# Kernel optimization log

Measured on AMD Instinct MI355X. Metric: run time of the kernel, lower is better.

## Reference

```python
import jax, jax.numpy as jnp
import numpy as np

BS, N, D, NC = 64, 512, 256, 4
REG = 0.5
N_ITER = 10
BIG = 1.0e9
LN_EPS = 1e-5


def _layer_norm(x, g, b):
    m = jnp.mean(x, axis=-1, keepdims=True)
    v = jnp.mean((x - m) ** 2, axis=-1, keepdims=True)
    return (x - m) * jax.lax.rsqrt(v + LN_EPS) * g + b


def _embed(x, W1, b1, g1, be1, W2, b2, g2, be2):
    h = _layer_norm(jax.nn.leaky_relu(x @ W1 + b1, 0.01), g1, be1)
    return _layer_norm(jax.nn.leaky_relu(h @ W2 + b2, 0.01), g2, be2)


def _one_hot_st(logits):
    # convert_one_hot(mode='max', hard=True, four_class=False, train): straight-through one-hot
    y = jax.nn.softmax(logits, axis=-1)
    y_hard = jax.nn.one_hot(jnp.argmax(y, axis=-1), logits.shape[-1], dtype=y.dtype)
    return jax.lax.stop_gradient(y_hard - y) + y


def _cdist(x, y):
    # torch.cdist p=2 (matmul form)
    sq = (jnp.sum(x * x, -1)[:, :, None] + jnp.sum(y * y, -1)[:, None, :]
          - 2.0 * jnp.einsum('bnd,bmd->bnm', x, y))
    return jnp.sqrt(jnp.maximum(sq, 0.0))


def _sinkhorn(a, b, C):
    # standard Sinkhorn-Knopp (POT sinkhorn_knopp), reg=REG, maxIter=N_ITER
    K = jnp.exp(-C / REG)
    def step(carry, _):
        u, v = carry
        v = b / (K.T @ u)
        u = a / (K @ v)
        return (u, v), None
    init = (jnp.full_like(a, 1.0 / a.shape[0]), jnp.full_like(b, 1.0 / b.shape[0]))
    (u, v), _ = jax.lax.scan(step, init, None, length=N_ITER)
    return u[:, None] * K * v[None, :]


def setup_inputs() -> dict:
    ks = jax.random.split(jax.random.key(0), 8)
    sc = 1.0 / np.sqrt(D)
    return {
        'case_A_logits': jax.random.normal(ks[0], (BS, N, NC), jnp.float32),
        'case_B_logits': jax.random.normal(ks[1], (BS, N, NC), jnp.float32),
        'case_A': jax.random.normal(ks[2], (BS, N, D), jnp.float32),
        'case_B': jax.random.normal(ks[3], (BS, N, D), jnp.float32),
        'relation_matrix': jax.random.uniform(ks[4], (BS, N, N), jnp.float32),
        'padding_mask_a': jnp.ones((BS, N), jnp.float32),
        'padding_mask_b': jnp.ones((BS, N), jnp.float32),
        'W1': jax.random.normal(ks[5], (D, D), jnp.float32) * sc,
        'b1': jnp.zeros((D,), jnp.float32),
        'g1': jnp.ones((D,), jnp.float32),
        'be1': jnp.zeros((D,), jnp.float32),
        'W2': jax.random.normal(ks[6], (D, D), jnp.float32) * sc,
        'b2': jnp.zeros((D,), jnp.float32),
        'g2': jnp.ones((D,), jnp.float32),
        'be2': jnp.zeros((D,), jnp.float32),
    }


def reference(case_A_logits, case_B_logits, case_A, case_B, relation_matrix,
              padding_mask_a, padding_mask_b,
              W1, b1, g1, be1, W2, b2, g2, be2):
    n = case_B_logits.shape[1]
    A1 = _one_hot_st(case_A_logits)                       # [bs, n, 4]
    B1 = _one_hot_st(case_B_logits)
    class_mask = jnp.einsum('bnc,bmc->bnm', A1, B1)       # [bs, n, n]
    pm = padding_mask_a[:, :, None] * padding_mask_b[:, None, :]
    pmv = -BIG * pm + BIG
    eA = _embed(case_A, W1, b1, g1, be1, W2, b2, g2, be2)
    eB = _embed(case_B, W1, b1, g1, be1, W2, b2, g2, be2)
    cost = _cdist(eA, eB)                                 # [bs, n, n]
    cost_class = cost + pmv                               # train path
    margin = jnp.full((n,), 1.0 / n, cost.dtype)
    plan = jax.vmap(lambda c: _sinkhorn(margin, margin, c))(cost_class)
    in_loss = jnp.mean(cost_class * class_mask * pm)
    out_loss = -jnp.mean(cost_class * (1.0 - class_mask) * pm)
    # simot branch: MSE criterion, simpercent=1.0 -> sim_mask all ones
    loss_raw = (plan * n - relation_matrix) ** 2
    sup_loss = jnp.sum(loss_raw * padding_mask_a[:, :, None]) / jnp.sum(padding_mask_a)
    return in_loss + out_loss + 10.0 * sup_loss
```

## Files before the change

### kernel.cpp

```cpp
#include <hip/hip_runtime.h>
#include <math.h>

#define BSZ 64
#define NPTS 512
#define DIM 256
#define MROWS 32768
#define TOTROWS 65536
#define BIGF 1.0e9f

typedef __bf16 bf16x8 __attribute__((ext_vector_type(8)));
typedef float  f32x4  __attribute__((ext_vector_type(4)));
typedef __attribute__((address_space(1))) const void* as1cv;
typedef __attribute__((address_space(3))) void* as3v;

#define KB_OFF    0ull
#define X_OFF     8388608ull
#define H_OFF     16777216ull
#define NORM_OFF  25165824ull
#define U_OFF     25231360ull
#define V_OFF     25264128ull
#define ARGA_OFF  25296896ull
#define ARGB_OFF  25329664ull
#define ACC_OFF   25362432ull
#define WT1_OFF   25362944ull
#define WT2_OFF   25395712ull

#define ACC_PA   0
#define ACC_IN   1
#define ACC_SUP  65
#define ACC_CNT  321

__device__ __forceinline__ float bf2f(unsigned short h) {
    return __uint_as_float(((unsigned int)h) << 16);
}
__device__ __forceinline__ unsigned short f2bf(float f) {
    unsigned int u = __float_as_uint(f);
    u = (u + 0x7FFFu + ((u >> 16) & 1u)) >> 16;
    return (unsigned short)u;
}

__device__ __forceinline__ float block_reduce_256(float val) {
    __shared__ float sh[4];
    int lane = threadIdx.x & 63;
    int wv = threadIdx.x >> 6;
    __syncthreads();
#pragma unroll
    for (int off = 32; off > 0; off >>= 1) val += __shfl_down(val, off, 64);
    if (lane == 0) sh[wv] = val;
    __syncthreads();
    float r = 0.f;
    if (wv == 0 && lane < 4) r = sh[lane];
    if (wv == 0) {
        r += __shfl_down(r, 2, 64);
        r += __shfl_down(r, 1, 64);
    }
    return r;
}

__device__ __forceinline__ void unpack8(uint4 w, float* k) {
    k[0] = __uint_as_float(w.x << 16);
    k[1] = __uint_as_float(w.x & 0xFFFF0000u);
    k[2] = __uint_as_float(w.y << 16);
    k[3] = __uint_as_float(w.y & 0xFFFF0000u);
    k[4] = __uint_as_float(w.z << 16);
    k[5] = __uint_as_float(w.z & 0xFFFF0000u);
    k[6] = __uint_as_float(w.w << 16);
    k[7] = __uint_as_float(w.w & 0xFFFF0000u);
}
__device__ __forceinline__ float dot8(const float* k, const float* vr) {
    float rs = k[0] * vr[0];
    rs = fmaf(k[1], vr[1], rs); rs = fmaf(k[2], vr[2], rs);
    rs = fmaf(k[3], vr[3], rs); rs = fmaf(k[4], vr[4], rs);
    rs = fmaf(k[5], vr[5], rs); rs = fmaf(k[6], vr[6], rs);
    return fmaf(k[7], vr[7], rs);
}

__device__ __forceinline__ float packed_reduce4(float p0, float p1, float p2, float p3, int l) {
    p0 += __shfl_xor(p0, 32, 64);
    p1 += __shfl_xor(p1, 32, 64);
    p2 += __shfl_xor(p2, 32, 64);
    p3 += __shfl_xor(p3, 32, 64);
    float m1 = (l & 32) ? p1 : p0;
    float m2 = (l & 32) ? p3 : p2;
    m1 += __shfl_xor(m1, 16, 64);
    m2 += __shfl_xor(m2, 16, 64);
    float s = (l & 16) ? m2 : m1;
    s += __shfl_xor(s, 8, 64);
    s += __shfl_xor(s, 4, 64);
    s += __shfl_xor(s, 2, 64);
    s += __shfl_xor(s, 1, 64);
    return s;
}
__device__ __forceinline__ float bcast_lane(float x, int lane) {
    return __uint_as_float((unsigned)__builtin_amdgcn_readlane((int)__float_as_uint(x), lane));
}

__global__ void zero_acc_kernel(float* acc, float* colsum) {
    int t = blockIdx.x * 256 + threadIdx.x;
    if (t < 512) acc[t] = 0.f;
    colsum[t] = 0.f;
}

__global__ __launch_bounds__(256) void argmax_pa_kernel(
    const float* __restrict__ la, const float* __restrict__ lb,
    const float* __restrict__ pa, int* __restrict__ argA, int* __restrict__ argB,
    float* __restrict__ acc) {
    int i = blockIdx.x * 256 + threadIdx.x;
    float4 a = *(const float4*)&la[(size_t)i * 4];
    float av[4] = {a.x, a.y, a.z, a.w};
    int ba = 0; float bv = av[0];
#pragma unroll
    for (int c = 1; c < 4; ++c) if (av[c] > bv) { bv = av[c]; ba = c; }
    argA[i] = ba;
    float4 b = *(const float4*)&lb[(size_t)i * 4];
    float bw[4] = {b.x, b.y, b.z, b.w};
    int bbi = 0; float bm = bw[0];
#pragma unroll
    for (int c = 1; c < 4; ++c) if (bw[c] > bm) { bm = bw[c]; bbi = c; }
    argB[i] = bbi;
    float p = pa[i];
#pragma unroll
    for (int off = 32; off > 0; off >>= 1) p += __shfl_down(p, off, 64);
    if ((threadIdx.x & 63) == 0) atomicAdd(&acc[ACC_PA], p);
}

__global__ __launch_bounds__(256) void cast_bf_kernel(
    const float* __restrict__ src, unsigned short* __restrict__ dst) {
    int tid = blockIdx.x * 256 + threadIdx.x;
#pragma unroll
    for (int k = 0; k < 4; ++k) {
        int i4 = tid + k * 524288;
        float4 v = *(const float4*)&src[(size_t)i4 * 4];
        ushort4 o;
        o.x = f2bf(v.x); o.y = f2bf(v.y); o.z = f2bf(v.z); o.w = f2bf(v.w);
        *(ushort4*)&dst[(size_t)i4 * 4] = o;
    }
}

__global__ __launch_bounds__(256) void cast_wt_kernel(
    const float* __restrict__ W, unsigned short* __restrict__ Wt) {
    __shared__ float tile[16][17];
    int tx = threadIdx.x & 15, ty = threadIdx.x >> 4;
    int bx = blockIdx.x, by = blockIdx.y;
    tile[ty][tx] = W[(size_t)(by * 16 + ty) * 256 + bx * 16 + tx];
    __syncthreads();
    Wt[(size_t)(bx * 16 + ty) * 256 + by * 16 + tx] = f2bf(tile[tx][ty]);
}

__global__ __launch_bounds__(256) void gemm_bf_kernel(
    const unsigned short* __restrict__ X, const unsigned short* __restrict__ Wt,
    unsigned short* __restrict__ Y) {
    __shared__ unsigned short Xs[64 * 40];
    __shared__ unsigned short Ws[256 * 40];
    const int t = threadIdx.x;
    const int L = t & 63, wv = t >> 6;
    const int q = L >> 4, n = L & 15;
    const size_t row0 = (size_t)blockIdx.x * 64;
    f32x4 acc[16];
#pragma unroll
    for (int nt = 0; nt < 16; ++nt) acc[nt] = (f32x4){0.f, 0.f, 0.f, 0.f};

    for (int k0 = 0; k0 < 256; k0 += 32) {
        {
            int r = t >> 2, seg = t & 3;
            *(uint4*)&Xs[r * 40 + seg * 8] =
                *(const uint4*)&X[(row0 + r) * 256 + k0 + seg * 8];
#pragma unroll
            for (int it = 0; it < 4; ++it) {
                int nn = (t >> 2) + it * 64;
                *(uint4*)&Ws[nn * 40 + seg * 8] =
                    *(const uint4*)&Wt[(size_t)nn * 256 + k0 + seg * 8];
            }
        }
        __syncthreads();
        bf16x8 av = *(const bf16x8*)&Xs[(wv * 16 + n) * 40 + q * 8];
#pragma unroll
        for (int nt = 0; nt < 16; ++nt) {
            bf16x8 bv = *(const bf16x8*)&Ws[(nt * 16 + n) * 40 + q * 8];
            acc[nt] = __builtin_amdgcn_mfma_f32_16x16x32_bf16(av, bv, acc[nt], 0, 0, 0);
        }
        __syncthreads();
    }
#pragma unroll
    for (int nt = 0; nt < 16; ++nt)
#pragma unroll
        for (int r = 0; r < 4; ++r) {
            size_t row = row0 + wv * 16 + q * 4 + r;
            Y[row * 256 + nt * 16 + n] = f2bf(acc[nt][r]);
        }
}

__global__ __launch_bounds__(256) void ln_bf_kernel(
    const unsigned short* __restrict__ Yin, unsigned short* __restrict__ Yout,
    const float* __restrict__ bias, const float* __restrict__ gam,
    const float* __restrict__ bet, float* __restrict__ norms) {
    int lane = threadIdx.x & 63;
    int wv = threadIdx.x >> 6;
    size_t row = (size_t)blockIdx.x * 4 + wv;
    ushort4 y4 = *(const ushort4*)&Yin[row * 256 + lane * 4];
    float4 b4 = *(const float4*)&bias[lane * 4];
    float h[4] = {bf2f(y4.x) + b4.x, bf2f(y4.y) + b4.y, bf2f(y4.z) + b4.z, bf2f(y4.w) + b4.w};
#pragma unroll
    for (int e = 0; e < 4; ++e) h[e] = h[e] >= 0.f ? h[e] : 0.01f * h[e];
    float s = h[0] + h[1] + h[2] + h[3];
    float sq = h[0] * h[0] + h[1] * h[1] + h[2] * h[2] + h[3] * h[3];
#pragma unroll
    for (int off = 32; off > 0; off >>= 1) {
        s += __shfl_down(s, off, 64);
        sq += __shfl_down(sq, off, 64);
    }
    s = __shfl(s, 0, 64); sq = __shfl(sq, 0, 64);
    float mean = s * (1.f / 256.f);
    float var = fmaxf(sq * (1.f / 256.f) - mean * mean, 0.f);
    float inv = rsqrtf(var + 1e-5f);
    float4 g4 = *(const float4*)&gam[lane * 4];
    float4 e4 = *(const float4*)&bet[lane * 4];
    float gv[4] = {g4.x, g4.y, g4.z, g4.w};
    float ev[4] = {e4.x, e4.y, e4.z, e4.w};
    ushort4 o4; float nr = 0.f;
    {
        unsigned short ob[4];
#pragma unroll
        for (int e = 0; e < 4; ++e) {
            float o = (h[e] - mean) * inv * gv[e] + ev[e];
            ob[e] = f2bf(o);
            float orr = bf2f(ob[e]);
            nr += orr * orr;
        }
        o4.x = ob[0]; o4.y = ob[1]; o4.z = ob[2]; o4.w = ob[3];
    }
    *(ushort4*)&Yout[row * 256 + lane * 4] = o4;
    if (norms) {
#pragma unroll
        for (int off = 32; off > 0; off >>= 1) nr += __shfl_down(nr, off, 64);
        if (lane == 0) norms[row] = nr;
    }
}

__global__ __launch_bounds__(256) void cost_mfma_kernel(
    const unsigned short* __restrict__ E, const float* __restrict__ norms,
    const int* __restrict__ argA, const int* __restrict__ argB,
    const float* __restrict__ pa, const float* __restrict__ pb,
    unsigned short* __restrict__ Kb16, float* __restrict__ acc,
    float* __restrict__ colsum) {
    __shared__ unsigned short As[64 * 256];
    __shared__ unsigned short Bs[64 * 256];
    const int t = threadIdx.x;
    const int L = t & 63, wv = t >> 6;
    const int q = L >> 4, n = L & 15;
    const int b = blockIdx.z;
    const int i0 = blockIdx.y * 64, j0 = blockIdx.x * 64;
    const unsigned short* eA = E + (size_t)b * 512 * 256;
    const unsigned short* eB = E + (size_t)(32768 + b * 512) * 256;

    {
        const int lrow = L >> 5;
        const int segp = L & 31;
#pragma unroll
        for (int j = 0; j < 8; ++j) {
            int row = wv * 16 + 2 * j + lrow;
            int sseg = segp ^ (row & 7);
            const unsigned short* ga = &eA[(size_t)(i0 + row) * 256 + sseg * 8];
            const unsigned short* gb = &eB[(size_t)(j0 + row) * 256 + sseg * 8];
            __builtin_amdgcn_global_load_lds((as1cv)ga, (as3v)&As[(wv * 16 + 2 * j) * 256],
                                             16, 0, 0);
            __builtin_amdgcn_global_load_lds((as1cv)gb, (as3v)&Bs[(wv * 16 + 2 * j) * 256],
                                             16, 0, 0);
        }
    }
    f32x4 dot[4];
#pragma unroll
    for (int nt = 0; nt < 4; ++nt) dot[nt] = (f32x4){0.f, 0.f, 0.f, 0.f};
    __syncthreads();

    const int rowa = wv * 16 + n;
    const int sw = n & 7;
#pragma unroll
    for (int c = 0; c < 8; ++c) {
        bf16x8 av = *(const bf16x8*)&As[rowa * 256 + (((c * 4 + q) ^ sw) * 8)];
#pragma unroll
        for (int nt = 0; nt < 4; ++nt) {
            int rowb = nt * 16 + n;
            bf16x8 bv = *(const bf16x8*)&Bs[rowb * 256 + (((c * 4 + q) ^ sw) * 8)];
            dot[nt] = __builtin_amdgcn_mfma_f32_16x16x32_bf16(av, bv, dot[nt], 0, 0, 0);
        }
    }

    int base_row = i0 + wv * 16 + q * 4;
    float nA[4], pAr[4]; int cA[4];
#pragma unroll
    for (int rr = 0; rr < 4; ++rr) {
        nA[rr] = norms[b * 512 + base_row + rr];
        pAr[rr] = pa[b * 512 + base_row + rr];
        cA[rr] = argA[b * 512 + base_row + rr];
    }
    float part = 0.f;
    float csnt[4];
#pragma unroll
    for (int nt = 0; nt < 4; ++nt) {
        int col = j0 + nt * 16 + n;
        float nB = norms[32768 + b * 512 + col];
        float pB = pb[b * 512 + col];
        int cB = argB[b * 512 + col];
        float cloc = 0.f;
#pragma unroll
        for (int rr = 0; rr < 4; ++rr) {
            float d2 = nA[rr] + nB - 2.f * dot[nt][rr];
            float c = sqrtf(fmaxf(d2, 0.f));
            float pm = pAr[rr] * pB;
            float cc = c + (BIGF - BIGF * pm);
            float sgn = (cA[rr] == cB) ? 1.f : -1.f;
            part += cc * sgn * pm;
            unsigned short kb = f2bf(expf(-2.f * cc));
            Kb16[((size_t)b * 512 + base_row + rr) * 512 + col] = kb;
            cloc += bf2f(kb);
        }
        csnt[nt] = cloc;
    }
    __syncthreads();
    float* red = (float*)As;
#pragma unroll
    for (int nt = 0; nt < 4; ++nt) {
        float sq2 = csnt[nt];
        sq2 += __shfl_xor(sq2, 16, 64);
        sq2 += __shfl_xor(sq2, 32, 64);
        if (L < 16) red[wv * 64 + nt * 16 + L] = sq2;
    }
    {
        float pw = part;
#pragma unroll
        for (int off = 32; off > 0; off >>= 1) pw += __shfl_down(pw, off, 64);
        if (L == 0) red[256 + wv] = pw;
    }
    __syncthreads();
    if (t < 64)
        atomicAdd(&colsum[(size_t)b * 512 + j0 + t],
                  red[t] + red[64 + t] + red[128 + t] + red[192 + t]);
    if (t == 0)
        atomicAdd(&acc[ACC_IN + b], red[256] + red[257] + red[258] + red[259]);
}

__global__ __launch_bounds__(1024) void sinkhorn_kernel(
    const unsigned short* __restrict__ Kb16, float* u, float* __restrict__ v) {
    const int b = blockIdx.x;
    const unsigned short* Kb = Kb16 + (size_t)b * 262144;
    __shared__ float vv[512];
    __shared__ float cp[16][512];
    const int t = threadIdx.x, wv = t >> 6, l = t & 63;
    const unsigned short* base = Kb + (size_t)(wv * 32) * 512 + l * 8;

    if (t < 512) vv[t] = 1.f / u[(size_t)b * 512 + t];
    __syncthreads();

    for (int it = 1; it <= 9; ++it) {
        float vr[8];
        *(f32x4*)&vr[0] = *(const f32x4*)&vv[l * 8];
        *(f32x4*)&vr[4] = *(const f32x4*)&vv[l * 8 + 4];
        float cs[8];
#pragma unroll
        for (int e = 0; e < 8; ++e) cs[e] = 0.f;
#pragma unroll 2
        for (int g = 0; g < 8; ++g) {
            const unsigned short* gb = base + (size_t)(g * 4) * 512;
            uint4 w0 = *(const uint4*)(gb);
            uint4 w1 = *(const uint4*)(gb + 512);
            uint4 w2 = *(const uint4*)(gb + 1024);
            uint4 w3 = *(const uint4*)(gb + 1536);
            float k0[8], k1[8], k2[8], k3[8];
            unpack8(w0, k0); unpack8(w1, k1); unpack8(w2, k2); unpack8(w3, k3);
            float p0 = dot8(k0, vr);
            float p1 = dot8(k1, vr);
            float p2 = dot8(k2, vr);
            float p3 = dot8(k3, vr);
            float s = packed_reduce4(p0, p1, p2, p3, l);
            float us = 0.001953125f * __builtin_amdgcn_rcpf(s);
            float uA = bcast_lane(us, 0);
            float uC = bcast_lane(us, 16);
            float uB = bcast_lane(us, 32);
            float uD = bcast_lane(us, 48);
#pragma unroll
            for (int e = 0; e < 8; ++e) {
                float c = fmaf(k0[e], uA, cs[e]);
                c = fmaf(k1[e], uB, c);
                c = fmaf(k2[e], uC, c);
                cs[e] = fmaf(k3[e], uD, c);
            }
        }
        *(f32x4*)&cp[wv][l * 8]     = *(f32x4*)&cs[0];
        *(f32x4*)&cp[wv][l * 8 + 4] = *(f32x4*)&cs[4];
        __syncthreads();
        if (t < 512) {
            float ss = 0.f;
#pragma unroll
            for (int k = 0; k < 16; ++k) ss += cp[k][t];
            vv[t] = (1.f / 512.f) / ss;
        }
        __syncthreads();
    }

    {
        float vr[8];
        *(f32x4*)&vr[0] = *(const f32x4*)&vv[l * 8];
        *(f32x4*)&vr[4] = *(const f32x4*)&vv[l * 8 + 4];
#pragma unroll 2
        for (int g = 0; g < 8; ++g) {
            const unsigned short* gb = base + (size_t)(g * 4) * 512;
            uint4 w0 = *(const uint4*)(gb);
            uint4 w1 = *(const uint4*)(gb + 512);
            uint4 w2 = *(const uint4*)(gb + 1024);
            uint4 w3 = *(const uint4*)(gb + 1536);
            float k0[8], k1[8], k2[8], k3[8];
            unpack8(w0, k0); unpack8(w1, k1); unpack8(w2, k2); unpack8(w3, k3);
            float p0 = dot8(k0, vr);
            float p1 = dot8(k1, vr);
            float p2 = dot8(k2, vr);
            float p3 = dot8(k3, vr);
            float s = packed_reduce4(p0, p1, p2, p3, l);
            if ((l & 15) == 0) {
                int g16 = l >> 4;
                int rof = ((g16 & 1) << 1) | (g16 >> 1);
                u[(size_t)b * 512 + wv * 32 + g * 4 + rof] = 0.001953125f / s;
            }
        }
    }
    if (t < 512) v[(size_t)b * 512 + t] = vv[t];
}

__global__ __launch_bounds__(256) void sup_kernel(
    const unsigned short* __restrict__ Kb16, const float* __restrict__ u,
    const float* __restrict__ v, const float* __restrict__ rel,
    const float* __restrict__ pa, float* __restrict__ acc) {
    const int nthreads = 4096 * 256;
    int tid = blockIdx.x * 256 + threadIdx.x;
    float part = 0.f;
#pragma unroll
    for (int k = 0; k < 4; ++k) {
        int i4 = tid + k * nthreads;
        int e = i4 * 4;
        int b = e >> 18;
        int i = (e >> 9) & 511;
        int j0 = e & 511;
        ushort4 K4 = *(const ushort4*)&Kb16[(size_t)i4 * 4];
        float4 r4 = *(const float4*)&rel[(size_t)i4 * 4];
        float4 v4 = *(const float4*)&v[b * 512 + j0];
        float ui = u[b * 512 + i] * 512.f;
        float pai = pa[b * 512 + i];
        float d0 = ui * bf2f(K4.x) * v4.x - r4.x;
        float d1 = ui * bf2f(K4.y) * v4.y - r4.y;
        float d2 = ui * bf2f(K4.z) * v4.z - r4.z;
        float d3 = ui * bf2f(K4.w) * v4.w - r4.w;
        part += (d0 * d0 + d1 * d1 + d2 * d2 + d3 * d3) * pai;
    }
    float tot = block_reduce_256(part);
    if (threadIdx.x == 0) atomicAdd(&acc[ACC_SUP + (blockIdx.x & 255)], tot);
}

__global__ __launch_bounds__(256) void final_kernel(const float* __restrict__ acc,
                                                    float* __restrict__ out) {
    int t = threadIdx.x;
    float vin = (t < 64) ? acc[ACC_IN + t] : 0.f;
    float sIn = block_reduce_256(vin);
    float vsup = acc[ACC_SUP + t];
    float sSup = block_reduce_256(vsup);
    if (t == 0)
        out[0] = sIn * (1.f / 16777216.f) + 10.f * sSup / acc[ACC_PA];
}

extern "C" void kernel_launch(void* const* d_in, const int* in_sizes, int n_in,
                              void* d_out, int out_size, void* d_ws, size_t ws_size,
                              hipStream_t stream) {
    const float* la  = (const float*)d_in[0];
    const float* lb  = (const float*)d_in[1];
    const float* xA  = (const float*)d_in[2];
    const float* xB  = (const float*)d_in[3];
    const float* rel = (const float*)d_in[4];
    const float* pa  = (const float*)d_in[5];
    const float* pb  = (const float*)d_in[6];
    const float* W1  = (const float*)d_in[7];
    const float* b1  = (const float*)d_in[8];
    const float* g1  = (const float*)d_in[9];
    const float* be1 = (const float*)d_in[10];
    const float* W2  = (const float*)d_in[11];
    const float* b2  = (const float*)d_in[12];
    const float* g2  = (const float*)d_in[13];
    const float* be2 = (const float*)d_in[14];
    float* out = (float*)d_out;

    float* ws = (float*)d_ws;
    unsigned short* Kb16 = (unsigned short*)(ws + KB_OFF);
    unsigned short* Xbf  = (unsigned short*)(ws + X_OFF);
    unsigned short* Hbf  = (unsigned short*)(ws + H_OFF);
    float* norms = ws + NORM_OFF;
    float* u     = ws + U_OFF;
    float* v     = ws + V_OFF;
    int* argA    = (int*)(ws + ARGA_OFF);
    int* argB    = (int*)(ws + ARGB_OFF);
    float* acc   = ws + ACC_OFF;
    unsigned short* Wt1 = (unsigned short*)(ws + WT1_OFF);
    unsigned short* Wt2 = (unsigned short*)(ws + WT2_OFF);

    zero_acc_kernel<<<128, 256, 0, stream>>>(acc, u);
    argmax_pa_kernel<<<128, 256, 0, stream>>>(la, lb, pa, argA, argB, acc);

    cast_bf_kernel<<<2048, 256, 0, stream>>>(xA, Xbf);
    cast_bf_kernel<<<2048, 256, 0, stream>>>(xB, Xbf + (size_t)MROWS * DIM);
    cast_wt_kernel<<<dim3(16, 16), 256, 0, stream>>>(W1, Wt1);
    cast_wt_kernel<<<dim3(16, 16), 256, 0, stream>>>(W2, Wt2);

    gemm_bf_kernel<<<1024, 256, 0, stream>>>(Xbf, Wt1, Kb16);
    ln_bf_kernel<<<16384, 256, 0, stream>>>(Kb16, Hbf, b1, g1, be1, nullptr);
    gemm_bf_kernel<<<1024, 256, 0, stream>>>(Hbf, Wt2, Kb16);
    ln_bf_kernel<<<16384, 256, 0, stream>>>(Kb16, Xbf, b2, g2, be2, norms);

    cost_mfma_kernel<<<dim3(8, 8, 64), 256, 0, stream>>>(Xbf, norms, argA, argB, pa, pb,
                                                         Kb16, acc, u);

    sinkhorn_kernel<<<64, 1024, 0, stream>>>(Kb16, u, v);

    sup_kernel<<<4096, 256, 0, stream>>>(Kb16, u, v, rel, pa, acc);
    final_kernel<<<1, 256, 0, stream>>>(acc, out);
}
```

Baseline: 401.9 us.

## Retile embedding GEMM with direct LDS loads and fuse final u-update into sup kernel

The embedding GEMM now tiles the output into 64x64 blocks over a 2D grid. Each block loads the full K=256 slice of A and B straight into XOR-swizzled shared memory with global_load_lds, replacing the k-looped staging that used padded shared arrays. The last u-update is dropped from the single-block-per-batch Sinkhorn kernel, and each sup_kernel block instead recomputes the row sums K·v for its own rows before evaluating the loss. This moves serial work off the low-parallelism Sinkhorn kernel and raises GEMM parallelism, at the cost of 64KB of LDS per GEMM block and A tiles being reloaded four times.

```diff
diff --git a/kernel.cpp b/kernel.cpp
--- a/kernel.cpp
+++ b/kernel.cpp
@@ -150,43 +150,50 @@
 __global__ __launch_bounds__(256) void gemm_bf_kernel(
     const unsigned short* __restrict__ X, const unsigned short* __restrict__ Wt,
     unsigned short* __restrict__ Y) {
-    __shared__ unsigned short Xs[64 * 40];
-    __shared__ unsigned short Ws[256 * 40];
+    __shared__ unsigned short As[64 * 256];
+    __shared__ unsigned short Bs[64 * 256];
     const int t = threadIdx.x;
     const int L = t & 63, wv = t >> 6;
     const int q = L >> 4, n = L & 15;
     const size_t row0 = (size_t)blockIdx.x * 64;
-    f32x4 acc[16];
-#pragma unroll
-    for (int nt = 0; nt < 16; ++nt) acc[nt] = (f32x4){0.f, 0.f, 0.f, 0.f};
-
-    for (int k0 = 0; k0 < 256; k0 += 32) {
-        {
-            int r = t >> 2, seg = t & 3;
-            *(uint4*)&Xs[r * 40 + seg * 8] =
-                *(const uint4*)&X[(row0 + r) * 256 + k0 + seg * 8];
-#pragma unroll
-            for (int it = 0; it < 4; ++it) {
-                int nn = (t >> 2) + it * 64;
-                *(uint4*)&Ws[nn * 40 + seg * 8] =
-                    *(const uint4*)&Wt[(size_t)nn * 256 + k0 + seg * 8];
-            }
-        }
-        __syncthreads();
-        bf16x8 av = *(const bf16x8*)&Xs[(wv * 16 + n) * 40 + q * 8];
-#pragma unroll
-        for (int nt = 0; nt < 16; ++nt) {
-            bf16x8 bv = *(const bf16x8*)&Ws[(nt * 16 + n) * 40 + q * 8];
-            acc[nt] = __builtin_amdgcn_mfma_f32_16x16x32_bf16(av, bv, acc[nt], 0, 0, 0);
-        }
-        __syncthreads();
-    }
-#pragma unroll
-    for (int nt = 0; nt < 16; ++nt)
+    const int n0 = blockIdx.y * 64;
+    {
+        const int lrow = L >> 5;
+        const int segp = L & 31;
+#pragma unroll
+        for (int j = 0; j < 8; ++j) {
+            int row = wv * 16 + 2 * j + lrow;
+            int sseg = segp ^ (row & 7);
+            const unsigned short* ga = &X[(row0 + row) * 256 + sseg * 8];
+            const unsigned short* gb = &Wt[(size_t)(n0 + row) * 256 + sseg * 8];
+            __builtin_amdgcn_global_load_lds((as1cv)ga, (as3v)&As[(wv * 16 + 2 * j) * 256],
+                                             16, 0, 0);
+            __builtin_amdgcn_global_load_lds((as1cv)gb, (as3v)&Bs[(wv * 16 + 2 * j) * 256],
+                                             16, 0, 0);
+        }
+    }
+    f32x4 dot[4];
+#pragma unroll
+    for (int nt = 0; nt < 4; ++nt) dot[nt] = (f32x4){0.f, 0.f, 0.f, 0.f};
+    __syncthreads();
+
+    const int rowa = wv * 16 + n;
+    const int sw = n & 7;
+#pragma unroll
+    for (int c = 0; c < 8; ++c) {
+        bf16x8 av = *(const bf16x8*)&As[rowa * 256 + (((c * 4 + q) ^ sw) * 8)];
+#pragma unroll
+        for (int nt = 0; nt < 4; ++nt) {
+            bf16x8 bv = *(const bf16x8*)&Bs[(nt * 16 + n) * 256 + (((c * 4 + q) ^ sw) * 8)];
+            dot[nt] = __builtin_amdgcn_mfma_f32_16x16x32_bf16(av, bv, dot[nt], 0, 0, 0);
+        }
+    }
+#pragma unroll
+    for (int nt = 0; nt < 4; ++nt)
 #pragma unroll
         for (int r = 0; r < 4; ++r) {
             size_t row = row0 + wv * 16 + q * 4 + r;
-            Y[row * 256 + nt * 16 + n] = f2bf(acc[nt][r]);
+            Y[row * 256 + n0 + nt * 16 + n] = f2bf(dot[nt][r]);
         }
 }
 
@@ -341,7 +348,8 @@
 }
 
 __global__ __launch_bounds__(1024) void sinkhorn_kernel(
-    const unsigned short* __restrict__ Kb16, float* u, float* __restrict__ v) {
+    const unsigned short* __restrict__ Kb16, const float* __restrict__ colsum,
+    float* __restrict__ v) {
     const int b = blockIdx.x;
     const unsigned short* Kb = Kb16 + (size_t)b * 262144;
     __shared__ float vv[512];
@@ -349,7 +357,7 @@
     const int t = threadIdx.x, wv = t >> 6, l = t & 63;
     const unsigned short* base = Kb + (size_t)(wv * 32) * 512 + l * 8;
 
-    if (t < 512) vv[t] = 1.f / u[(size_t)b * 512 + t];
+    if (t < 512) vv[t] = 1.f / colsum[(size_t)b * 512 + t];
     __syncthreads();
 
     for (int it = 1; it <= 9; ++it) {
@@ -397,62 +405,50 @@
         }
         __syncthreads();
     }
-
-    {
-        float vr[8];
-        *(f32x4*)&vr[0] = *(const f32x4*)&vv[l * 8];
-        *(f32x4*)&vr[4] = *(const f32x4*)&vv[l * 8 + 4];
-#pragma unroll 2
-        for (int g = 0; g < 8; ++g) {
-            const unsigned short* gb = base + (size_t)(g * 4) * 512;
-            uint4 w0 = *(const uint4*)(gb);
-            uint4 w1 = *(const uint4*)(gb + 512);
-            uint4 w2 = *(const uint4*)(gb + 1024);
-            uint4 w3 = *(const uint4*)(gb + 1536);
-            float k0[8], k1[8], k2[8], k3[8];
-            unpack8(w0, k0); unpack8(w1, k1); unpack8(w2, k2); unpack8(w3, k3);
-            float p0 = dot8(k0, vr);
-            float p1 = dot8(k1, vr);
-            float p2 = dot8(k2, vr);
-            float p3 = dot8(k3, vr);
-            float s = packed_reduce4(p0, p1, p2, p3, l);
-            if ((l & 15) == 0) {
-                int g16 = l >> 4;
-                int rof = ((g16 & 1) << 1) | (g16 >> 1);
-                u[(size_t)b * 512 + wv * 32 + g * 4 + rof] = 0.001953125f / s;
-            }
-        }
-    }
     if (t < 512) v[(size_t)b * 512 + t] = vv[t];
 }
 
 __global__ __launch_bounds__(256) void sup_kernel(
-    const unsigned short* __restrict__ Kb16, const float* __restrict__ u,
-    const float* __restrict__ v, const float* __restrict__ rel,
-    const float* __restrict__ pa, float* __restrict__ acc) {
-    const int nthreads = 4096 * 256;
-    int tid = blockIdx.x * 256 + threadIdx.x;
+    const unsigned short* __restrict__ Kb16, const float* __restrict__ v,
+    const float* __restrict__ rel, const float* __restrict__ pa,
+    float* __restrict__ acc) {
+    const int b = blockIdx.x >> 6;
+    const int rg = blockIdx.x & 63;
+    const int t = threadIdx.x;
+    const int h = t >> 5;
+    const int c = t & 31;
+    const int row = rg * 8 + h;
+    const unsigned int* kp =
+        (const unsigned int*)(Kb16 + ((size_t)b * 512 + row) * 512 + c * 16);
+    uint4 kw0 = *(const uint4*)(kp);
+    uint4 kw1 = *(const uint4*)(kp + 4);
+    float k[16];
+    unpack8(kw0, k); unpack8(kw1, k + 8);
+    float vr[16];
+    *(f32x4*)&vr[0]  = *(const f32x4*)&v[b * 512 + c * 16];
+    *(f32x4*)&vr[4]  = *(const f32x4*)&v[b * 512 + c * 16 + 4];
+    *(f32x4*)&vr[8]  = *(const f32x4*)&v[b * 512 + c * 16 + 8];
+    *(f32x4*)&vr[12] = *(const f32x4*)&v[b * 512 + c * 16 + 12];
+    float rs = 0.f;
+#pragma unroll
+    for (int e = 0; e < 16; ++e) rs = fmaf(k[e], vr[e], rs);
+#pragma unroll
+    for (int off = 16; off > 0; off >>= 1) rs += __shfl_xor(rs, off, 32);
+    float inv = 1.f / rs;
     float part = 0.f;
-#pragma unroll
-    for (int k = 0; k < 4; ++k) {
-        int i4 = tid + k * nthreads;
-        int e = i4 * 4;
-        int b = e >> 18;
-        int i = (e >> 9) & 511;
-        int j0 = e & 511;
-        ushort4 K4 = *(const ushort4*)&Kb16[(size_t)i4 * 4];
-        float4 r4 = *(const float4*)&rel[(size_t)i4 * 4];
-        float4 v4 = *(const float4*)&v[b * 512 + j0];
-        float ui = u[b * 512 + i] * 512.f;
-        float pai = pa[b * 512 + i];
-        float d0 = ui * bf2f(K4.x) * v4.x - r4.x;
-        float d1 = ui * bf2f(K4.y) * v4.y - r4.y;
-        float d2 = ui * bf2f(K4.z) * v4.z - r4.z;
-        float d3 = ui * bf2f(K4.w) * v4.w - r4.w;
-        part += (d0 * d0 + d1 * d1 + d2 * d2 + d3 * d3) * pai;
-    }
+    const float* rp = &rel[((size_t)b * 512 + row) * 512 + c * 16];
+#pragma unroll
+    for (int e = 0; e < 16; e += 4) {
+        float4 r4 = *(const float4*)(rp + e);
+        float d0 = k[e]     * vr[e]     * inv - r4.x;
+        float d1 = k[e + 1] * vr[e + 1] * inv - r4.y;
+        float d2 = k[e + 2] * vr[e + 2] * inv - r4.z;
+        float d3 = k[e + 3] * vr[e + 3] * inv - r4.w;
+        part += d0 * d0 + d1 * d1 + d2 * d2 + d3 * d3;
+    }
+    part *= pa[b * 512 + row];
     float tot = block_reduce_256(part);
-    if (threadIdx.x == 0) atomicAdd(&acc[ACC_SUP + (blockIdx.x & 255)], tot);
+    if (t == 0) atomicAdd(&acc[ACC_SUP + (blockIdx.x & 255)], tot);
 }
 
 __global__ __launch_bounds__(256) void final_kernel(const float* __restrict__ acc,
@@ -507,9 +503,9 @@
     cast_wt_kernel<<<dim3(16, 16), 256, 0, stream>>>(W1, Wt1);
     cast_wt_kernel<<<dim3(16, 16), 256, 0, stream>>>(W2, Wt2);
 
-    gemm_bf_kernel<<<1024, 256, 0, stream>>>(Xbf, Wt1, Kb16);
+    gemm_bf_kernel<<<dim3(1024, 4), 256, 0, stream>>>(Xbf, Wt1, Kb16);
     ln_bf_kernel<<<16384, 256, 0, stream>>>(Kb16, Hbf, b1, g1, be1, nullptr);
-    gemm_bf_kernel<<<1024, 256, 0, stream>>>(Hbf, Wt2, Kb16);
+    gemm_bf_kernel<<<dim3(1024, 4), 256, 0, stream>>>(Hbf, Wt2, Kb16);
     ln_bf_kernel<<<16384, 256, 0, stream>>>(Kb16, Xbf, b2, g2, be2, norms);
 
     cost_mfma_kernel<<<dim3(8, 8, 64), 256, 0, stream>>>(Xbf, norms, argA, argB, pa, pb,
@@ -517,6 +513,6 @@
 
     sinkhorn_kernel<<<64, 1024, 0, stream>>>(Kb16, u, v);
 
-    sup_kernel<<<4096, 256, 0, stream>>>(Kb16, u, v, rel, pa, acc);
+    sup_kernel<<<4096, 256, 0, stream>>>(Kb16, v, rel, pa, acc);
     final_kernel<<<1, 256, 0, stream>>>(acc, out);
 }
```

Measured after the change: 400.1 us. Within noise of the previous version (-0.4%).
